# Optimization experiments

Measured on AMD Instinct MI355X. Metric: run time of the kernel, lower is better.

## Reference

```python
import jax, jax.numpy as jnp
import numpy as np

N_NODES, N_EDGES = 100000, 1600000
D_IN, D_HID, D_OUT = 128, 128, 64


def setup_inputs() -> dict:
    key = jax.random.key(0)
    k = jax.random.split(key, 6)
    x = jax.random.normal(k[0], (N_NODES, D_IN), dtype=jnp.float32)
    edge_index = jax.random.randint(k[1], (2, N_EDGES), 0, N_NODES, dtype=jnp.int32)
    # GCNConv params: W stored as [in, out] for right-multiply, glorot-ish scale
    W1 = jax.random.normal(k[2], (D_IN, D_HID), dtype=jnp.float32) * (1.0 / np.sqrt(D_IN))
    b1 = jnp.zeros((D_HID,), dtype=jnp.float32)
    W2 = jax.random.normal(k[3], (D_HID, D_OUT), dtype=jnp.float32) * (1.0 / np.sqrt(D_HID))
    b2 = jnp.zeros((D_OUT,), dtype=jnp.float32)
    return {"x": x, "edge_index": edge_index, "W1": W1, "b1": b1, "W2": W2, "b2": b2}


def reference(x, edge_index, W1, b1, W2, b2):
    N = x.shape[0]
    loops = jnp.arange(N, dtype=edge_index.dtype)
    src = jnp.concatenate([edge_index[0], loops])  # [E+N]
    dst = jnp.concatenate([edge_index[1], loops])  # [E+N]
    # symmetric GCN normalization (deg over targets, incl. self loops)
    deg = jax.ops.segment_sum(jnp.ones_like(dst, dtype=x.dtype), dst, num_segments=N)
    dinv = jnp.where(deg > 0, jax.lax.rsqrt(deg), 0.0)
    norm = dinv[src] * dinv[dst]  # [E+N]

    def gcn(h, W, b):
        h = h @ W                         # [N, out]
        msg = h[src] * norm[:, None]      # gather + scale, [E+N, out]
        return jax.ops.segment_sum(msg, dst, num_segments=N) + b

    h = jax.nn.relu(gcn(x, W1, b1))  # Dropout is identity in eval
    return gcn(h, W2, b2)
```

## Files before the change

### kernel.cpp

```cpp
#include <hip/hip_runtime.h>


#define D_IN  128
#define D_HID 128
#define D_OUT 64
#define NBSHIFT 9

typedef short short8 __attribute__((ext_vector_type(8)));
typedef float floatx4 __attribute__((ext_vector_type(4)));

__device__ __forceinline__ unsigned short f2bf(float f) {
    unsigned int u = __float_as_uint(f);
    u += 0x7fffu + ((u >> 16) & 1u);
    return (unsigned short)(u >> 16);
}
__device__ __forceinline__ float bf2f(unsigned short h) {
    return __uint_as_float((unsigned int)h << 16);
}
__device__ __forceinline__ float bf_lo(unsigned int u) { return __uint_as_float(u << 16); }
__device__ __forceinline__ float bf_hi(unsigned int u) { return __uint_as_float(u & 0xffff0000u); }


__global__ __launch_bounds__(256) void k_zero_int(int* __restrict__ p, int n) {
    int i = blockIdx.x * 256 + threadIdx.x;
    if (i < n) p[i] = 0;
}

__global__ __launch_bounds__(256) void k_bhist(const int* __restrict__ dst,
                                               int* __restrict__ bcnt, int E, int NB) {
    __shared__ int h[256];
    const int t = threadIdx.x;
    h[t] = 0;
    __syncthreads();
    const int base = blockIdx.x * 8192;
#pragma unroll
    for (int k = 0; k < 32; ++k) {
        int e = base + k * 256 + t;
        if (e < E) atomicAdd(&h[dst[e] >> NBSHIFT], 1);
    }
    __syncthreads();
    if (t < NB && h[t]) atomicAdd(&bcnt[t], h[t]);
}

__global__ __launch_bounds__(256) void k_bscan(const int* __restrict__ bcnt,
                                               int* __restrict__ bbase,
                                               int* __restrict__ bcur, int NB, int E) {
    __shared__ int ls[256];
    const int t = threadIdx.x;
    int v = (t < NB) ? bcnt[t] : 0;
    ls[t] = v;
    __syncthreads();
    for (int off = 1; off < 256; off <<= 1) {
        int y = (t >= off) ? ls[t - off] : 0;
        __syncthreads();
        ls[t] += y;
        __syncthreads();
    }
    if (t < NB) {
        bbase[t] = ls[t] - v;
        bcur[t]  = ls[t] - v;
    }
    if (t == 0) bbase[NB] = E;
}

__global__ __launch_bounds__(256) void k_bin(const int* __restrict__ src,
                                             const int* __restrict__ dst,
                                             int2* __restrict__ ebuf,
                                             int* __restrict__ bcur, int E, int NB) {
    __shared__ int h[256];
    __shared__ int basep[256];
    const int t = threadIdx.x;
    h[t] = 0;
    __syncthreads();
    const int base = blockIdx.x * 4096;
    int s[16], d[16];
#pragma unroll
    for (int k = 0; k < 16; ++k) {
        int e = base + k * 256 + t;
        bool v = e < E;
        s[k] = v ? src[e] : 0;
        d[k] = v ? dst[e] : -1;
        if (v) atomicAdd(&h[d[k] >> NBSHIFT], 1);
    }
    __syncthreads();
    if (t < NB && h[t]) basep[t] = atomicAdd(&bcur[t], h[t]);
    __syncthreads();
    h[t] = 0;
    __syncthreads();
#pragma unroll
    for (int k = 0; k < 16; ++k) {
        if (d[k] >= 0) {
            int b = d[k] >> NBSHIFT;
            int r = atomicAdd(&h[b], 1);
            ebuf[basep[b] + r] = make_int2(s[k], d[k]);
        }
    }
}

__global__ __launch_bounds__(256) void k_bfill(const int2* __restrict__ ebuf,
                                               const int* __restrict__ bbase,
                                               int* __restrict__ csr,
                                               int* __restrict__ rowstart,
                                               float* __restrict__ dinv,
                                               int N, int NB, int E) {
    __shared__ int cnt[512];
    __shared__ int pref[512];
    __shared__ int tsum[256];
    const int t = threadIdx.x;
    const int b = blockIdx.x;
    const int nb0 = b << NBSHIFT;
    const int NN = min(512, N - nb0);
    const int e0 = bbase[b], e1 = bbase[b + 1];

    cnt[t] = 0;
    cnt[t + 256] = 0;
    __syncthreads();
    for (int e = e0 + t; e < e1; e += 256)
        atomicAdd(&cnt[ebuf[e].y - nb0], 1);
    __syncthreads();

    int a0 = cnt[2 * t], a1 = cnt[2 * t + 1];
    tsum[t] = a0 + a1;
    __syncthreads();
    for (int off = 1; off < 256; off <<= 1) {
        int y = (t >= off) ? tsum[t - off] : 0;
        __syncthreads();
        tsum[t] += y;
        __syncthreads();
    }
    int excl = tsum[t] - (a0 + a1);
    pref[2 * t] = excl;
    pref[2 * t + 1] = excl + a0;
    __syncthreads();

    for (int nl = t; nl < NN; nl += 256) {
        rowstart[nb0 + nl] = e0 + pref[nl];
        dinv[nb0 + nl] = rsqrtf((float)(cnt[nl] + 1));
    }
    if (b == NB - 1 && t == 0) rowstart[N] = E;
    __syncthreads();

    for (int e = e0 + t; e < e1; e += 256) {
        int2 ed = ebuf[e];
        int r = atomicAdd(&pref[ed.y - nb0], 1);
        csr[e0 + r] = ed.x;
    }
}

__global__ void k_zero_pad(unsigned short* __restrict__ h1b,
                           unsigned short* __restrict__ h2b, int N) {
    int t = threadIdx.x;
    if (t < 128) h1b[(size_t)N * 128 + t] = 0;
    if (t < 64)  h2b[(size_t)N * 64 + t] = 0;
}


template <int DOUT_>
__global__ __launch_bounds__(256) void k_wsplit(const float* __restrict__ W,
                                                unsigned short* __restrict__ Ws) {
    constexpr int NCT = DOUT_ / 16;
    constexpr int HALF = 4 * NCT * 64 * 8;
    int id = blockIdx.x * 256 + threadIdx.x;
    if (id >= HALF) return;
    int i = id & 7;
    int lane = (id >> 3) & 63;
    int ctkt = id >> 9;
    int ct = ctkt % NCT, kt = ctkt / NCT;
    int k = kt * 32 + ((lane >> 4) << 3) + i;
    int n = ct * 16 + (lane & 15);
    float v = W[(size_t)k * DOUT_ + n];
    unsigned short h = f2bf(v);
    Ws[id] = h;
    Ws[HALF + id] = f2bf(v - bf2f(h));
}


template <int DOUT_>
__global__ __launch_bounds__(256) void mfma_gemm(const float* __restrict__ X,
                                                 const unsigned short* __restrict__ Wsplit,
                                                 const float* __restrict__ dinv,
                                                 unsigned short* __restrict__ Hb,
                                                 int N) {
    constexpr int NCT = DOUT_ / 16;
    constexpr int HALF = 4 * NCT * 64 * 8;
    __shared__ unsigned short lds[2 * HALF];

    const int t = threadIdx.x;
    {
        const int4* s4 = (const int4*)Wsplit;
        int4* d4 = (int4*)lds;
        constexpr int NV = 2 * HALF / 8;
        for (int i = t; i < NV; i += 256) d4[i] = s4[i];
    }
    __syncthreads();

    const int wave = t >> 6, lane = t & 63;
    const int grow = blockIdx.x * 64 + wave * 16 + (lane & 15);
    const int rowc = min(grow, N - 1);
    const int kl = (lane >> 4) << 3;

    floatx4 acc[NCT];
#pragma unroll
    for (int c = 0; c < NCT; ++c) acc[c] = (floatx4)0.f;

#pragma unroll
    for (int kt = 0; kt < 4; ++kt) {
        const float* xp = X + (size_t)rowc * 128 + kt * 32 + kl;
        float4 a0 = *(const float4*)xp;
        float4 a1 = *(const float4*)(xp + 4);
        float xs[8] = {a0.x, a0.y, a0.z, a0.w, a1.x, a1.y, a1.z, a1.w};
        short8 ah, al;
#pragma unroll
        for (int i = 0; i < 8; ++i) {
            unsigned short h = f2bf(xs[i]);
            ah[i] = (short)h;
            al[i] = (short)f2bf(xs[i] - bf2f(h));
        }
#pragma unroll
        for (int c = 0; c < NCT; ++c) {
            const int off = ((kt * NCT + c) * 64 + lane) * 8;
            short8 bh = *(const short8*)&lds[off];
            short8 bl = *(const short8*)&lds[HALF + off];
            acc[c] = __builtin_amdgcn_mfma_f32_16x16x32_bf16(ah, bh, acc[c], 0, 0, 0);
            acc[c] = __builtin_amdgcn_mfma_f32_16x16x32_bf16(al, bh, acc[c], 0, 0, 0);
            acc[c] = __builtin_amdgcn_mfma_f32_16x16x32_bf16(ah, bl, acc[c], 0, 0, 0);
        }
    }

    const int orow = blockIdx.x * 64 + wave * 16 + ((lane >> 4) << 2);
#pragma unroll
    for (int r = 0; r < 4; ++r) {
        int gr = orow + r;
        if (gr < N) {
            float dn = dinv[gr];
#pragma unroll
            for (int c = 0; c < NCT; ++c)
                Hb[(size_t)gr * DOUT_ + c * 16 + (lane & 15)] = f2bf(acc[c][r] * dn);
        }
    }
}


__global__ __launch_bounds__(256) void agg1_kernel(const uint4* __restrict__ H4,
                                                   const int* __restrict__ rowstart,
                                                   const int* __restrict__ csr_src,
                                                   const float* __restrict__ dinv,
                                                   const float* __restrict__ bias,
                                                   float* __restrict__ out, int N) {
    const int t = threadIdx.x;
    const int wave = t >> 6, lane = t & 63;
    const int g = lane >> 4, gl = lane & 15;
    const int n = blockIdx.x * 16 + wave * 4 + g;
    const bool live = n < N;
    const int e0 = live ? rowstart[n] : 0;
    const int e1 = live ? rowstart[n + 1] : 0;
    const int deg = e1 - e0;
    int m = deg;
    m = max(m, __shfl_xor(m, 16));
    m = max(m, __shfl_xor(m, 32));

    float acc[8] = {0.f, 0.f, 0.f, 0.f, 0.f, 0.f, 0.f, 0.f};
    for (int eb = 0; eb < m; eb += 16) {
        int s_l = (eb + gl < deg) ? csr_src[e0 + eb + gl] : N;
        for (int j = 0; j < 16 && eb + j < m; j += 4) {
            int sj[4]; uint4 u[4];
#pragma unroll
            for (int q = 0; q < 4; ++q) sj[q] = __shfl(s_l, (g << 4) | (j + q));
#pragma unroll
            for (int q = 0; q < 4; ++q) u[q] = H4[(size_t)sj[q] * 16 + gl];
#pragma unroll
            for (int q = 0; q < 4; ++q) {
                acc[0] += bf_lo(u[q].x); acc[1] += bf_hi(u[q].x);
                acc[2] += bf_lo(u[q].y); acc[3] += bf_hi(u[q].y);
                acc[4] += bf_lo(u[q].z); acc[5] += bf_hi(u[q].z);
                acc[6] += bf_lo(u[q].w); acc[7] += bf_hi(u[q].w);
            }
        }
    }
    uint4 us = H4[(size_t)(live ? n : N) * 16 + gl];
    acc[0] += bf_lo(us.x); acc[1] += bf_hi(us.x);
    acc[2] += bf_lo(us.y); acc[3] += bf_hi(us.y);
    acc[4] += bf_lo(us.z); acc[5] += bf_hi(us.z);
    acc[6] += bf_lo(us.w); acc[7] += bf_hi(us.w);

    if (live) {
        const float dn = dinv[n];
        float4 o0, o1;
        o0.x = fmaxf(fmaf(acc[0], dn, bias[gl * 8 + 0]), 0.f);
        o0.y = fmaxf(fmaf(acc[1], dn, bias[gl * 8 + 1]), 0.f);
        o0.z = fmaxf(fmaf(acc[2], dn, bias[gl * 8 + 2]), 0.f);
        o0.w = fmaxf(fmaf(acc[3], dn, bias[gl * 8 + 3]), 0.f);
        o1.x = fmaxf(fmaf(acc[4], dn, bias[gl * 8 + 4]), 0.f);
        o1.y = fmaxf(fmaf(acc[5], dn, bias[gl * 8 + 5]), 0.f);
        o1.z = fmaxf(fmaf(acc[6], dn, bias[gl * 8 + 6]), 0.f);
        o1.w = fmaxf(fmaf(acc[7], dn, bias[gl * 8 + 7]), 0.f);
        float* op = out + (size_t)n * 128 + gl * 8;
        *reinterpret_cast<float4*>(op) = o0;
        *reinterpret_cast<float4*>(op + 4) = o1;
    }
}

__global__ __launch_bounds__(256) void agg2_kernel(const uint4* __restrict__ H4,
                                                   const int* __restrict__ rowstart,
                                                   const int* __restrict__ csr_src,
                                                   const float* __restrict__ dinv,
                                                   const float* __restrict__ bias,
                                                   float* __restrict__ out, int N) {
    const int t = threadIdx.x;
    const int wave = t >> 6, lane = t & 63;
    const int g = lane >> 3, gl = lane & 7;
    const int n = blockIdx.x * 32 + wave * 8 + g;
    const bool live = n < N;
    const int e0 = live ? rowstart[n] : 0;
    const int e1 = live ? rowstart[n + 1] : 0;
    const int deg = e1 - e0;
    int m = deg;
    m = max(m, __shfl_xor(m, 8));
    m = max(m, __shfl_xor(m, 16));
    m = max(m, __shfl_xor(m, 32));

    float acc[8] = {0.f, 0.f, 0.f, 0.f, 0.f, 0.f, 0.f, 0.f};
    for (int eb = 0; eb < m; eb += 8) {
        int s_l = (eb + gl < deg) ? csr_src[e0 + eb + gl] : N;
        for (int j = 0; j < 8 && eb + j < m; j += 4) {
            int sj[4]; uint4 u[4];
#pragma unroll
            for (int q = 0; q < 4; ++q) sj[q] = __shfl(s_l, (g << 3) | (j + q));
#pragma unroll
            for (int q = 0; q < 4; ++q) u[q] = H4[(size_t)sj[q] * 8 + gl];
#pragma unroll
            for (int q = 0; q < 4; ++q) {
                acc[0] += bf_lo(u[q].x); acc[1] += bf_hi(u[q].x);
                acc[2] += bf_lo(u[q].y); acc[3] += bf_hi(u[q].y);
                acc[4] += bf_lo(u[q].z); acc[5] += bf_hi(u[q].z);
                acc[6] += bf_lo(u[q].w); acc[7] += bf_hi(u[q].w);
            }
        }
    }
    uint4 us = H4[(size_t)(live ? n : N) * 8 + gl];
    acc[0] += bf_lo(us.x); acc[1] += bf_hi(us.x);
    acc[2] += bf_lo(us.y); acc[3] += bf_hi(us.y);
    acc[4] += bf_lo(us.z); acc[5] += bf_hi(us.z);
    acc[6] += bf_lo(us.w); acc[7] += bf_hi(us.w);

    if (live) {
        const float dn = dinv[n];
        float4 o0, o1;
        o0.x = fmaf(acc[0], dn, bias[gl * 8 + 0]);
        o0.y = fmaf(acc[1], dn, bias[gl * 8 + 1]);
        o0.z = fmaf(acc[2], dn, bias[gl * 8 + 2]);
        o0.w = fmaf(acc[3], dn, bias[gl * 8 + 3]);
        o1.x = fmaf(acc[4], dn, bias[gl * 8 + 4]);
        o1.y = fmaf(acc[5], dn, bias[gl * 8 + 5]);
        o1.z = fmaf(acc[6], dn, bias[gl * 8 + 6]);
        o1.w = fmaf(acc[7], dn, bias[gl * 8 + 7]);
        float* op = out + (size_t)n * 64 + gl * 8;
        *reinterpret_cast<float4*>(op) = o0;
        *reinterpret_cast<float4*>(op + 4) = o1;
    }
}


extern "C" void kernel_launch(void* const* d_in, const int* in_sizes, int n_in,
                              void* d_out, int out_size, void* d_ws, size_t ws_size,
                              hipStream_t stream) {
    const float* x  = (const float*)d_in[0];
    const int*   ei = (const int*)d_in[1];
    const float* W1 = (const float*)d_in[2];
    const float* b1 = (const float*)d_in[3];
    const float* W2 = (const float*)d_in[4];
    const float* b2 = (const float*)d_in[5];
    float* out = (float*)d_out;

    const int N = in_sizes[0] / D_IN;
    const int E = in_sizes[1] / 2;
    const int* src = ei;
    const int* dst = ei + E;
    const int NB = (N + 511) >> NBSHIFT;

    char* w = (char*)d_ws;
    auto alloc = [&](size_t bytes) {
        char* p = w;
        w += (bytes + 255) & ~(size_t)255;
        return p;
    };
    int*   rowstart  = (int*)alloc((size_t)(N + 1) * 4);
    float* dinv      = (float*)alloc((size_t)N * 4);
    int*   csr       = (int*)alloc((size_t)E * 4);
    unsigned short* h1b = (unsigned short*)alloc((size_t)(N + 1) * D_HID * 2);
    unsigned short* h2b = (unsigned short*)alloc((size_t)(N + 1) * D_OUT * 2);
    float* hg        = (float*)alloc((size_t)N * D_HID * 4);
    int*   bcnt      = (int*)alloc((size_t)NB * 4);
    int*   bbase     = (int*)alloc((size_t)(NB + 1) * 4);
    int*   bcur      = (int*)alloc((size_t)NB * 4);
    unsigned short* w1s = (unsigned short*)alloc(2 * 4 * (D_HID / 16) * 64 * 8 * 2);
    unsigned short* w2s = (unsigned short*)alloc(2 * 4 * (D_OUT / 16) * 64 * 8 * 2);
    int2*  ebuf      = (int2*)hg;

    k_zero_int<<<1, 256, 0, stream>>>(bcnt, NB);
    k_bhist<<<(E + 8191) / 8192, 256, 0, stream>>>(dst, bcnt, E, NB);
    k_bscan<<<1, 256, 0, stream>>>(bcnt, bbase, bcur, NB, E);
    k_bin<<<(E + 4095) / 4096, 256, 0, stream>>>(src, dst, ebuf, bcur, E, NB);
    k_bfill<<<NB, 256, 0, stream>>>(ebuf, bbase, csr, rowstart, dinv, N, NB, E);
    k_zero_pad<<<1, 128, 0, stream>>>(h1b, h2b, N);
    k_wsplit<D_HID><<<(4 * (D_HID / 16) * 64 * 8 + 255) / 256, 256, 0, stream>>>(W1, w1s);
    k_wsplit<D_OUT><<<(4 * (D_OUT / 16) * 64 * 8 + 255) / 256, 256, 0, stream>>>(W2, w2s);

    mfma_gemm<D_HID><<<(N + 63) / 64, 256, 0, stream>>>(x, w1s, dinv, h1b, N);
    agg1_kernel<<<(N + 15) / 16, 256, 0, stream>>>((const uint4*)h1b, rowstart, csr,
                                                   dinv, b1, hg, N);
    mfma_gemm<D_OUT><<<(N + 63) / 64, 256, 0, stream>>>(hg, w2s, dinv, h2b, N);
    agg2_kernel<<<(N + 31) / 32, 256, 0, stream>>>((const uint4*)h2b, rowstart, csr,
                                                   dinv, b2, out, N);
}
```

Baseline: 213.7 us.

## Split layer-1 aggregation into XCD-mapped feature halves and store hidden as bf16

The first aggregation kernel now processes each node's 128 features in two 64-wide halves, handled by different blocks. Block indices are mapped so each half is served by a fixed group of XCDs, with the aim that each XCD's L2 holds only half of the gathered feature table. The hidden activations are written as bf16 instead of fp32, and a new GEMM variant reads bf16 input directly, which halves that intermediate traffic. The gather loops in both aggregation kernels are unrolled to issue eight loads per batch. The costs are an extra bf16 rounding of the hidden layer, duplicated index reads across the two halves, and a reliance on round-robin block-to-XCD scheduling.

```diff
diff --git a/kernel.cpp b/kernel.cpp
--- a/kernel.cpp
+++ b/kernel.cpp
@@ -241,43 +241,102 @@
 }
 
 
+template <int DOUT_>
+__global__ __launch_bounds__(256) void mfma_gemm_b(const unsigned short* __restrict__ Xb,
+                                                   const unsigned short* __restrict__ Wsplit,
+                                                   const float* __restrict__ dinv,
+                                                   unsigned short* __restrict__ Hb,
+                                                   int N) {
+    constexpr int NCT = DOUT_ / 16;
+    constexpr int HALF = 4 * NCT * 64 * 8;
+    __shared__ unsigned short lds[2 * HALF];
+
+    const int t = threadIdx.x;
+    {
+        const int4* s4 = (const int4*)Wsplit;
+        int4* d4 = (int4*)lds;
+        constexpr int NV = 2 * HALF / 8;
+        for (int i = t; i < NV; i += 256) d4[i] = s4[i];
+    }
+    __syncthreads();
+
+    const int wave = t >> 6, lane = t & 63;
+    const int grow = blockIdx.x * 64 + wave * 16 + (lane & 15);
+    const int rowc = min(grow, N - 1);
+    const int kl = (lane >> 4) << 3;
+
+    floatx4 acc[NCT];
+#pragma unroll
+    for (int c = 0; c < NCT; ++c) acc[c] = (floatx4)0.f;
+
+#pragma unroll
+    for (int kt = 0; kt < 4; ++kt) {
+        short8 ah = *(const short8*)(Xb + (size_t)rowc * 128 + kt * 32 + kl);
+#pragma unroll
+        for (int c = 0; c < NCT; ++c) {
+            const int off = ((kt * NCT + c) * 64 + lane) * 8;
+            short8 bh = *(const short8*)&lds[off];
+            short8 bl = *(const short8*)&lds[HALF + off];
+            acc[c] = __builtin_amdgcn_mfma_f32_16x16x32_bf16(ah, bh, acc[c], 0, 0, 0);
+            acc[c] = __builtin_amdgcn_mfma_f32_16x16x32_bf16(ah, bl, acc[c], 0, 0, 0);
+        }
+    }
+
+    const int orow = blockIdx.x * 64 + wave * 16 + ((lane >> 4) << 2);
+#pragma unroll
+    for (int r = 0; r < 4; ++r) {
+        int gr = orow + r;
+        if (gr < N) {
+            float dn = dinv[gr];
+#pragma unroll
+            for (int c = 0; c < NCT; ++c)
+                Hb[(size_t)gr * DOUT_ + c * 16 + (lane & 15)] = f2bf(acc[c][r] * dn);
+        }
+    }
+}
+
+
 __global__ __launch_bounds__(256) void agg1_kernel(const uint4* __restrict__ H4,
                                                    const int* __restrict__ rowstart,
                                                    const int* __restrict__ csr_src,
                                                    const float* __restrict__ dinv,
                                                    const float* __restrict__ bias,
-                                                   float* __restrict__ out, int N) {
+                                                   unsigned short* __restrict__ outb,
+                                                   int N, int NBK) {
+    const int xcd = blockIdx.x & 7;
+    const int ch  = xcd >> 2;
+    const int nb  = (blockIdx.x >> 3) * 4 + (xcd & 3);
+    if (nb >= NBK) return;
     const int t = threadIdx.x;
     const int wave = t >> 6, lane = t & 63;
-    const int g = lane >> 4, gl = lane & 15;
-    const int n = blockIdx.x * 16 + wave * 4 + g;
+    const int g = lane >> 3, gl = lane & 7;
+    const int n = nb * 32 + wave * 8 + g;
     const bool live = n < N;
     const int e0 = live ? rowstart[n] : 0;
-    const int e1 = live ? rowstart[n + 1] : 0;
-    const int deg = e1 - e0;
+    const int deg = live ? rowstart[n + 1] - e0 : 0;
     int m = deg;
+    m = max(m, __shfl_xor(m, 8));
     m = max(m, __shfl_xor(m, 16));
     m = max(m, __shfl_xor(m, 32));
 
+    const int cb = ch * 8;
     float acc[8] = {0.f, 0.f, 0.f, 0.f, 0.f, 0.f, 0.f, 0.f};
-    for (int eb = 0; eb < m; eb += 16) {
+    for (int eb = 0; eb < m; eb += 8) {
         int s_l = (eb + gl < deg) ? csr_src[e0 + eb + gl] : N;
-        for (int j = 0; j < 16 && eb + j < m; j += 4) {
-            int sj[4]; uint4 u[4];
-#pragma unroll
-            for (int q = 0; q < 4; ++q) sj[q] = __shfl(s_l, (g << 4) | (j + q));
-#pragma unroll
-            for (int q = 0; q < 4; ++q) u[q] = H4[(size_t)sj[q] * 16 + gl];
-#pragma unroll
-            for (int q = 0; q < 4; ++q) {
-                acc[0] += bf_lo(u[q].x); acc[1] += bf_hi(u[q].x);
-                acc[2] += bf_lo(u[q].y); acc[3] += bf_hi(u[q].y);
-                acc[4] += bf_lo(u[q].z); acc[5] += bf_hi(u[q].z);
-                acc[6] += bf_lo(u[q].w); acc[7] += bf_hi(u[q].w);
-            }
-        }
-    }
-    uint4 us = H4[(size_t)(live ? n : N) * 16 + gl];
+        int sj[8]; uint4 u[8];
+#pragma unroll
+        for (int q = 0; q < 8; ++q) sj[q] = __shfl(s_l, (g << 3) | q);
+#pragma unroll
+        for (int q = 0; q < 8; ++q) u[q] = H4[(size_t)sj[q] * 16 + cb + gl];
+#pragma unroll
+        for (int q = 0; q < 8; ++q) {
+            acc[0] += bf_lo(u[q].x); acc[1] += bf_hi(u[q].x);
+            acc[2] += bf_lo(u[q].y); acc[3] += bf_hi(u[q].y);
+            acc[4] += bf_lo(u[q].z); acc[5] += bf_hi(u[q].z);
+            acc[6] += bf_lo(u[q].w); acc[7] += bf_hi(u[q].w);
+        }
+    }
+    uint4 us = H4[(size_t)(live ? n : N) * 16 + cb + gl];
     acc[0] += bf_lo(us.x); acc[1] += bf_hi(us.x);
     acc[2] += bf_lo(us.y); acc[3] += bf_hi(us.y);
     acc[4] += bf_lo(us.z); acc[5] += bf_hi(us.z);
@@ -285,18 +344,13 @@
 
     if (live) {
         const float dn = dinv[n];
-        float4 o0, o1;
-        o0.x = fmaxf(fmaf(acc[0], dn, bias[gl * 8 + 0]), 0.f);
-        o0.y = fmaxf(fmaf(acc[1], dn, bias[gl * 8 + 1]), 0.f);
-        o0.z = fmaxf(fmaf(acc[2], dn, bias[gl * 8 + 2]), 0.f);
-        o0.w = fmaxf(fmaf(acc[3], dn, bias[gl * 8 + 3]), 0.f);
-        o1.x = fmaxf(fmaf(acc[4], dn, bias[gl * 8 + 4]), 0.f);
-        o1.y = fmaxf(fmaf(acc[5], dn, bias[gl * 8 + 5]), 0.f);
-        o1.z = fmaxf(fmaf(acc[6], dn, bias[gl * 8 + 6]), 0.f);
-        o1.w = fmaxf(fmaf(acc[7], dn, bias[gl * 8 + 7]), 0.f);
-        float* op = out + (size_t)n * 128 + gl * 8;
-        *reinterpret_cast<float4*>(op) = o0;
-        *reinterpret_cast<float4*>(op + 4) = o1;
+        const float* bp = bias + ch * 64 + gl * 8;
+        unsigned short o[8];
+#pragma unroll
+        for (int j = 0; j < 8; ++j)
+            o[j] = f2bf(fmaxf(fmaf(acc[j], dn, bp[j]), 0.f));
+        *reinterpret_cast<int4*>(&outb[(size_t)n * 128 + ch * 64 + gl * 8]) =
+            *reinterpret_cast<const int4*>(o);
     }
 }
 
@@ -322,19 +376,17 @@
     float acc[8] = {0.f, 0.f, 0.f, 0.f, 0.f, 0.f, 0.f, 0.f};
     for (int eb = 0; eb < m; eb += 8) {
         int s_l = (eb + gl < deg) ? csr_src[e0 + eb + gl] : N;
-        for (int j = 0; j < 8 && eb + j < m; j += 4) {
-            int sj[4]; uint4 u[4];
-#pragma unroll
-            for (int q = 0; q < 4; ++q) sj[q] = __shfl(s_l, (g << 3) | (j + q));
-#pragma unroll
-            for (int q = 0; q < 4; ++q) u[q] = H4[(size_t)sj[q] * 8 + gl];
-#pragma unroll
-            for (int q = 0; q < 4; ++q) {
-                acc[0] += bf_lo(u[q].x); acc[1] += bf_hi(u[q].x);
-                acc[2] += bf_lo(u[q].y); acc[3] += bf_hi(u[q].y);
-                acc[4] += bf_lo(u[q].z); acc[5] += bf_hi(u[q].z);
-                acc[6] += bf_lo(u[q].w); acc[7] += bf_hi(u[q].w);
-            }
+        int sj[8]; uint4 u[8];
+#pragma unroll
+        for (int q = 0; q < 8; ++q) sj[q] = __shfl(s_l, (g << 3) | q);
+#pragma unroll
+        for (int q = 0; q < 8; ++q) u[q] = H4[(size_t)sj[q] * 8 + gl];
+#pragma unroll
+        for (int q = 0; q < 8; ++q) {
+            acc[0] += bf_lo(u[q].x); acc[1] += bf_hi(u[q].x);
+            acc[2] += bf_lo(u[q].y); acc[3] += bf_hi(u[q].y);
+            acc[4] += bf_lo(u[q].z); acc[5] += bf_hi(u[q].z);
+            acc[6] += bf_lo(u[q].w); acc[7] += bf_hi(u[q].w);
         }
     }
     uint4 us = H4[(size_t)(live ? n : N) * 8 + gl];
@@ -389,13 +441,13 @@
     int*   csr       = (int*)alloc((size_t)E * 4);
     unsigned short* h1b = (unsigned short*)alloc((size_t)(N + 1) * D_HID * 2);
     unsigned short* h2b = (unsigned short*)alloc((size_t)(N + 1) * D_OUT * 2);
-    float* hg        = (float*)alloc((size_t)N * D_HID * 4);
+    unsigned short* hgb = (unsigned short*)alloc((size_t)N * D_HID * 2);
     int*   bcnt      = (int*)alloc((size_t)NB * 4);
     int*   bbase     = (int*)alloc((size_t)(NB + 1) * 4);
     int*   bcur      = (int*)alloc((size_t)NB * 4);
     unsigned short* w1s = (unsigned short*)alloc(2 * 4 * (D_HID / 16) * 64 * 8 * 2);
     unsigned short* w2s = (unsigned short*)alloc(2 * 4 * (D_OUT / 16) * 64 * 8 * 2);
-    int2*  ebuf      = (int2*)hg;
+    int2*  ebuf      = (int2*)hgb;
 
     k_zero_int<<<1, 256, 0, stream>>>(bcnt, NB);
     k_bhist<<<(E + 8191) / 8192, 256, 0, stream>>>(dst, bcnt, E, NB);
@@ -407,9 +459,11 @@
     k_wsplit<D_OUT><<<(4 * (D_OUT / 16) * 64 * 8 + 255) / 256, 256, 0, stream>>>(W2, w2s);
 
     mfma_gemm<D_HID><<<(N + 63) / 64, 256, 0, stream>>>(x, w1s, dinv, h1b, N);
-    agg1_kernel<<<(N + 15) / 16, 256, 0, stream>>>((const uint4*)h1b, rowstart, csr,
-                                                   dinv, b1, hg, N);
-    mfma_gemm<D_OUT><<<(N + 63) / 64, 256, 0, stream>>>(hg, w2s, dinv, h2b, N);
+
+    const int NBK = (N + 31) / 32;
+    agg1_kernel<<<((NBK + 3) / 4) * 8, 256, 0, stream>>>((const uint4*)h1b, rowstart, csr,
+                                                         dinv, b1, hgb, N, NBK);
+    mfma_gemm_b<D_OUT><<<(N + 63) / 64, 256, 0, stream>>>(hgb, w2s, dinv, h2b, N);
     agg2_kernel<<<(N + 31) / 32, 256, 0, stream>>>((const uint4*)h2b, rowstart, csr,
                                                    dinv, b2, out, N);
 }
```

Result: faster. 198.0 us (-7.3%).
